# Kernel optimization log

Measured on AMD Instinct MI355X. Metric: run time of the kernel, lower is better.

Reference implementation:

```python
import jax, jax.numpy as jnp
import numpy as np

B, N, T, F_IN, K, NUM_CLASSES = 32, 62, 1024, 5, 9, 3
CH = [F_IN, 32, 64, 128]
STRIDES = [1, 2, 1]
EPS = 1e-5  # torch InstanceNorm2d default eps


def setup_inputs() -> dict:
    key = jax.random.key(0)
    ks = jax.random.split(key, 32)
    ctr = [0]
    def nxt():
        k = ks[ctr[0]]; ctr[0] += 1; return k
    def nrm(shape, fan_in):
        return jax.random.normal(nxt(), shape, dtype=jnp.float32) / np.float32(np.sqrt(fan_in))
    inp = {}
    inp["x"] = jax.random.normal(nxt(), (B, N, T, F_IN), dtype=jnp.float32)
    # frozen learned graph: symmetric, non-negative, sparse-ish, zero diagonal
    a = jax.random.uniform(nxt(), (N, N), dtype=jnp.float32)
    a = jnp.maximum(jnp.tanh(a + a.T), 0.0)
    a = jnp.where(a > 0.8, a, 0.0)
    inp["adj"] = a * (1.0 - jnp.eye(N, dtype=jnp.float32))
    for i in range(3):
        cin, cout = CH[i], CH[i + 1]
        inp[f"gcn_w{i}"] = nrm((cin, cout), cin)
        inp[f"gcn_b{i}"] = jnp.zeros((cout,), jnp.float32)
        inp[f"conv_w{i}"] = nrm((cout, cout, 1, K), cout * K)
        inp[f"conv_b{i}"] = jnp.zeros((cout,), jnp.float32)
        inp[f"res_w{i}"] = nrm((cout, cin, 1, 1), cin)
        inp[f"res_b{i}"] = jnp.zeros((cout,), jnp.float32)
    inp["attn_w1"] = nrm((128, 64), 128)
    inp["attn_b1"] = jnp.zeros((64,), jnp.float32)
    inp["attn_w2"] = nrm((64, 1), 64)
    inp["attn_b2"] = jnp.zeros((1,), jnp.float32)
    inp["fc_w"] = nrm((128, NUM_CLASSES), 128)
    inp["fc_b"] = jnp.zeros((NUM_CLASSES,), jnp.float32)
    return inp


def _instance_norm(x):
    # InstanceNorm2d, affine=False: normalize per (sample, channel) over (node, time)
    m = jnp.mean(x, axis=(2, 3), keepdims=True)
    v = jnp.mean(jnp.square(x - m), axis=(2, 3), keepdims=True)
    return (x - m) * jax.lax.rsqrt(v + EPS)


def _conv(x, w, b, stride, pad):
    y = jax.lax.conv_general_dilated(
        x, w, window_strides=(1, stride), padding=[(0, 0), (pad, pad)],
        dimension_numbers=("NCHW", "OIHW", "NCHW"))
    return y + b[None, :, None, None]


def _block(x, a_norm, wg, bg, wc, bc, wr, br, stride):
    # residual 1x1 conv (always present: in!=out for every block here)
    res = _conv(x, wr, br, stride, 0)
    # GCNConv over all (batch, time) slices at once: A_norm @ (X W) + b
    y = jnp.einsum("bfnt,fo->bont", x, wg)
    y = jnp.einsum("mn,bont->bomt", a_norm, y) + bg[None, :, None, None]
    # TCN: IN -> ReLU -> Conv(1,K) -> IN -> ReLU (dropout = identity in eval)
    y = jax.nn.relu(_instance_norm(y))
    y = _conv(y, wc, bc, stride, (K - 1) // 2)
    y = jax.nn.relu(_instance_norm(y))
    return jax.nn.relu(y + res)


def _forward(x, adj, params, attn_w1, attn_b1, attn_w2, attn_b2, fc_w, fc_b):
    # symmetric GCN normalization with self loops (PyG gcn_norm on dense support)
    a_hat = adj + jnp.eye(N, dtype=adj.dtype)
    d = jnp.sum(a_hat, axis=1)
    dinv = jnp.where(d > 0, jax.lax.rsqrt(jnp.maximum(d, EPS)), 0.0)
    a_norm = dinv[:, None] * a_hat * dinv[None, :]
    h = jnp.transpose(x, (0, 3, 1, 2))  # (B, F, N, T)
    for i in range(3):
        h = _block(h, a_norm, *params[i], STRIDES[i])
    h = jnp.transpose(jnp.mean(h, axis=2), (0, 2, 1))  # (B, T', 128)
    hid = jnp.tanh(h @ attn_w1 + attn_b1)
    score = (hid @ attn_w2)[..., 0] + attn_b2[0]      # (B, T')
    w = jax.nn.softmax(score, axis=1)
    feat = jnp.einsum("btf,bt->bf", h, w)
    logits = feat @ fc_w + fc_b
    return logits, adj


def reference(x, adj,
              gcn_w0, gcn_b0, conv_w0, conv_b0, res_w0, res_b0,
              gcn_w1, gcn_b1, conv_w1, conv_b1, res_w1, res_b1,
              gcn_w2, gcn_b2, conv_w2, conv_b2, res_w2, res_b2,
              attn_w1, attn_b1, attn_w2, attn_b2, fc_w, fc_b):
    params = [
        (gcn_w0, gcn_b0, conv_w0, conv_b0, res_w0, res_b0),
        (gcn_w1, gcn_b1, conv_w1, conv_b1, res_w1, res_b1),
        (gcn_w2, gcn_b2, conv_w2, conv_b2, res_w2, res_b2),
    ]
    return _forward(x, adj, params, attn_w1, attn_b1, attn_w2, attn_b2, fc_w, fc_b)
```

## Files before the change

kernel.cpp:

```cpp
#include <hip/hip_runtime.h>


#define NN 62
#define KK 9

typedef short s16x8 __attribute__((ext_vector_type(8)));
typedef float f32x4 __attribute__((ext_vector_type(4)));

__device__ __forceinline__ unsigned short f2bf(float f) {
  unsigned u = __builtin_bit_cast(unsigned, f);
  u += 0x7FFF + ((u >> 16) & 1);
  return (unsigned short)(u >> 16);
}
__device__ __forceinline__ float bf2f(unsigned short u) {
  unsigned v = ((unsigned)u) << 16;
  return __builtin_bit_cast(float, v);
}
__device__ __forceinline__ ushort4 pack4(float4 a) {
  return (ushort4){f2bf(a.x), f2bf(a.y), f2bf(a.z), f2bf(a.w)};
}

__global__ __launch_bounds__(256) void k_prep(const float* __restrict__ adj,
                                              float* __restrict__ a_norm,
                                              float* __restrict__ out_adj) {
  __shared__ float dinv[NN];
  int tid = threadIdx.x;
  if (tid < NN) {
    float s = 1.0f;
    for (int n = 0; n < NN; n++) s += adj[tid * NN + n];
    dinv[tid] = (s > 0.f) ? rsqrtf(fmaxf(s, 1e-5f)) : 0.f;
  }
  __syncthreads();
  for (int idx = tid; idx < NN * NN; idx += 256) {
    int m = idx / NN, n = idx - m * NN;
    float ah = adj[idx] + ((m == n) ? 1.f : 0.f);
    a_norm[idx] = dinv[m] * ah * dinv[n];
    out_adj[idx] = adj[idx];
  }
}

__global__ __launch_bounds__(256) void k_an(const float* __restrict__ a_norm,
                                            unsigned short* __restrict__ anf) {
  int idx = blockIdx.x * 256 + threadIdx.x;
  if (idx >= 4096) return;
  int j = idx & 7;
  int l = (idx >> 3) & 63;
  int rest = idx >> 9;
  int cb = rest & 1;
  int ob = rest >> 1;
  int m = ob * 16 + (l & 15);
  int n = cb * 32 + (l >> 4) * 8 + j;
  anf[idx] = (m < NN && n < NN) ? f2bf(a_norm[m * NN + n]) : (unsigned short)0;
}

__global__ __launch_bounds__(256) void k_wt(const float* __restrict__ wc,
                                            unsigned short* __restrict__ wf, int C) {
  int stride = gridDim.x * blockDim.x;
  int total = KK * C * C;
  int nCB = C / 32;
  for (int idx = blockIdx.x * blockDim.x + threadIdx.x; idx < total; idx += stride) {
    int j = idx & 7;
    int l = (idx >> 3) & 63;
    int rest = idx >> 9;
    int cb = rest % nCB;
    int rest2 = rest / nCB;
    int ob = rest2 % (C / 16);
    int k = rest2 / (C / 16);
    int o = ob * 16 + (l & 15);
    int ci = cb * 32 + (l >> 4) * 8 + j;
    wf[idx] = f2bf(wc[((size_t)o * C + ci) * KK + k]);
  }
}

__global__ __launch_bounds__(256) void k_wg(const float* __restrict__ gw,
                                            unsigned short* __restrict__ wgf,
                                            int CIN, int COUT, int KPAD) {
  int total = (COUT / 16) * (KPAD / 32) * 512;
  int stride = gridDim.x * blockDim.x;
  for (int idx = blockIdx.x * blockDim.x + threadIdx.x; idx < total; idx += stride) {
    int j = idx & 7;
    int l = (idx >> 3) & 63;
    int rest = idx >> 9;
    int cb = rest % (KPAD / 32);
    int ob = rest / (KPAD / 32);
    int o = ob * 16 + (l & 15);
    int f = cb * 32 + (l >> 4) * 8 + j;
    wgf[idx] = (f < CIN) ? f2bf(gw[(size_t)f * COUT + o]) : (unsigned short)0;
  }
}

__global__ __launch_bounds__(256) void k_wr(const float* __restrict__ wr,
                                            unsigned short* __restrict__ wrf,
                                            int CIN, int COUT, int KPAD) {
  int total = (COUT / 16) * (KPAD / 32) * 512;
  int stride = gridDim.x * blockDim.x;
  for (int idx = blockIdx.x * blockDim.x + threadIdx.x; idx < total; idx += stride) {
    int j = idx & 7;
    int l = (idx >> 3) & 63;
    int rest = idx >> 9;
    int cb = rest % (KPAD / 32);
    int ob = rest / (KPAD / 32);
    int o = ob * 16 + (l & 15);
    int f = cb * 32 + (l >> 4) * 8 + j;
    wrf[idx] = (f < CIN) ? f2bf(wr[(size_t)o * CIN + f]) : (unsigned short)0;
  }
}

__global__ __launch_bounds__(256) void k_xcast(const float* __restrict__ x,
                                               unsigned short* __restrict__ xb, int b0) {
  constexpr int TT2 = 256, TIN = 1024, CIN = 5;
  __shared__ float xt[TT2 * CIN];
  int t0 = blockIdx.x * TT2, n = blockIdx.y, bl = blockIdx.z;
  int tid = threadIdx.x;
  const float* xp = x + ((size_t)((b0 + bl) * NN + n) * TIN + t0) * CIN;
  for (int i = tid; i < TT2 * CIN; i += 256) xt[i] = xp[i];
  __syncthreads();
  for (int i = tid; i < CIN * TT2; i += 256) {
    int f = i / TT2, tl = i - f * TT2;
    xb[((size_t)bl * CIN + f) * NN * TIN + (size_t)n * TIN + t0 + tl] = f2bf(xt[tl * CIN + f]);
  }
}

template <int CIN, int TIN>
__global__ __launch_bounds__(256) void k_spatmma(const unsigned short* __restrict__ in,
                                                 const unsigned short* __restrict__ anf,
                                                 unsigned short* __restrict__ xs) {
  constexpr int BT = 256;
  constexpr int CP = 72;
  constexpr int BNP = BT + 8;
  constexpr int ZTSZ = BT * CP;
  constexpr int WLSZ = 4096;
  constexpr int OTSZ = 64 * BNP;
  constexpr int SH = (ZTSZ + WLSZ > OTSZ) ? ZTSZ + WLSZ : OTSZ;
  __shared__ unsigned short sh[SH];
  unsigned short* zt = sh;
  unsigned short* wl = sh + ZTSZ;

  int t0 = blockIdx.x * BT;
  int f = blockIdx.y;
  int bl = blockIdx.z;
  int tid = threadIdx.x;

  for (int i = tid * 4; i < WLSZ; i += 1024)
    *reinterpret_cast<ushort4*>(&wl[i]) = *reinterpret_cast<const ushort4*>(&anf[i]);

  const unsigned short* ib = in + ((size_t)bl * CIN + f) * (size_t)NN * TIN;
  for (int i = tid * 4; i < 64 * BT; i += 1024) {
    int n = i / BT, tl = i - n * BT;
    ushort4 u = {0, 0, 0, 0};
    if (n < NN) u = *reinterpret_cast<const ushort4*>(&ib[(size_t)n * TIN + t0 + tl]);
    unsigned short vv[4] = {u.x, u.y, u.z, u.w};
    int xo = ((tl >> 2) & 7) << 3;
#pragma unroll
    for (int j = 0; j < 4; j++) zt[(tl + j) * CP + (n ^ xo)] = vv[j];
  }
  __syncthreads();

  int w = tid >> 6;
  int lane = tid & 63;
  int lm = lane & 15, kh = lane >> 4;
  int col0 = w * 64;

  f32x4 acc[4][4];
#pragma unroll
  for (int mf = 0; mf < 4; mf++)
#pragma unroll
    for (int nf = 0; nf < 4; nf++) acc[mf][nf] = (f32x4){0.f, 0.f, 0.f, 0.f};

#pragma unroll
  for (int cb = 0; cb < 2; cb++) {
    s16x8 a[4], b[4];
#pragma unroll
    for (int mf = 0; mf < 4; mf++)
      a[mf] = *reinterpret_cast<const s16x8*>(&wl[(mf * 2 + cb) * 512 + lane * 8]);
#pragma unroll
    for (int nf = 0; nf < 4; nf++) {
      int col = col0 + nf * 16 + lm;
      int off = (cb * 32 + kh * 8) ^ (((col >> 2) & 7) << 3);
      b[nf] = *reinterpret_cast<const s16x8*>(&zt[col * CP + off]);
    }
#pragma unroll
    for (int mf = 0; mf < 4; mf++)
#pragma unroll
      for (int nf = 0; nf < 4; nf++)
        acc[mf][nf] = __builtin_amdgcn_mfma_f32_16x16x32_bf16(a[mf], b[nf], acc[mf][nf], 0, 0, 0);
  }

  __syncthreads();
  unsigned short* ot = sh;
#pragma unroll
  for (int mf = 0; mf < 4; mf++)
#pragma unroll
    for (int nf = 0; nf < 4; nf++) {
      int col = col0 + nf * 16 + lm;
#pragma unroll
      for (int rr = 0; rr < 4; rr++) {
        int m = mf * 16 + kh * 4 + rr;
        ot[m * BNP + col] = f2bf(acc[mf][nf][rr]);
      }
    }
  __syncthreads();
  for (int i = tid * 4; i < NN * BT; i += 1024) {
    int m = i / BT, col = i - m * BT;
    ushort4 v = *reinterpret_cast<const ushort4*>(&ot[m * BNP + col]);
    *reinterpret_cast<ushort4*>(&xs[(((size_t)bl * CIN + f) * NN + m) * TIN + t0 + col]) = v;
  }
}

template <int CIN, int COUT, int TIN>
__global__ __launch_bounds__(256) void k_wmixmma(const unsigned short* __restrict__ xs,
                                                 const unsigned short* __restrict__ wgf,
                                                 unsigned short* __restrict__ y,
                                                 float* __restrict__ part) {
  constexpr int S = NN * TIN;
  constexpr int KPAD = (CIN <= 32) ? 32 : 64;
  constexpr int CP = KPAD + 8;
  constexpr int BN = (COUT >= 128) ? 128 : 256;
  constexpr int BNP = BN + 8;
  constexpr int WM = (COUT >= 64) ? 2 : 1;
  constexpr int WN = 4 / WM;
  constexpr int MF = COUT / (16 * WM);
  constexpr int NF = BN / (16 * WN);
  constexpr int XM = (KPAD == 32) ? 3 : 7;
  constexpr int ZTSZ = BN * CP;
  constexpr int WLSZ = COUT * KPAD;
  constexpr int OTSZ = COUT * BNP;
  constexpr int SH = (ZTSZ + WLSZ > OTSZ) ? ZTSZ + WLSZ : OTSZ;
  __shared__ unsigned short sh[SH];
  unsigned short* zt = sh;
  unsigned short* wl = sh + ZTSZ;

  int s0 = blockIdx.x * BN;
  int bl = blockIdx.y;
  int tid = threadIdx.x;

  for (int i = tid * 4; i < WLSZ; i += 1024)
    *reinterpret_cast<ushort4*>(&wl[i]) = *reinterpret_cast<const ushort4*>(&wgf[i]);

  const unsigned short* xb = xs + (size_t)bl * CIN * S;
  for (int i = tid * 4; i < KPAD * BN; i += 1024) {
    int f = i / BN, sl = i - (i / BN) * BN;
    ushort4 u = {0, 0, 0, 0};
    if (f < CIN) u = *reinterpret_cast<const ushort4*>(&xb[(size_t)f * S + s0 + sl]);
    unsigned short vv[4] = {u.x, u.y, u.z, u.w};
#pragma unroll
    for (int j = 0; j < 4; j++) {
      int s_ = sl + j;
      zt[s_ * CP + (f ^ ((((s_) >> 2) & XM) << 3))] = vv[j];
    }
  }
  __syncthreads();

  int w = tid >> 6;
  int lane = tid & 63;
  int lm = lane & 15, kh = lane >> 4;
  int o0w = (w / WN) * (COUT / WM);
  int col0 = (w % WN) * (BN / WN);
  int obBase = o0w >> 4;

  f32x4 acc[MF][NF];
#pragma unroll
  for (int mf = 0; mf < MF; mf++)
#pragma unroll
    for (int nf = 0; nf < NF; nf++) acc[mf][nf] = (f32x4){0.f, 0.f, 0.f, 0.f};

#pragma unroll
  for (int cb = 0; cb < KPAD / 32; cb++) {
    s16x8 a[MF], b[NF];
#pragma unroll
    for (int mf = 0; mf < MF; mf++)
      a[mf] = *reinterpret_cast<const s16x8*>(&wl[((obBase + mf) * (KPAD / 32) + cb) * 512 + lane * 8]);
#pragma unroll
    for (int nf = 0; nf < NF; nf++) {
      int col = col0 + nf * 16 + lm;
      int off = (cb * 32 + kh * 8) ^ (((col >> 2) & XM) << 3);
      b[nf] = *reinterpret_cast<const s16x8*>(&zt[col * CP + off]);
    }
#pragma unroll
    for (int mf = 0; mf < MF; mf++)
#pragma unroll
      for (int nf = 0; nf < NF; nf++)
        acc[mf][nf] = __builtin_amdgcn_mfma_f32_16x16x32_bf16(a[mf], b[nf], acc[mf][nf], 0, 0, 0);
  }

  __syncthreads();
  unsigned short* ot = sh;
#pragma unroll
  for (int mf = 0; mf < MF; mf++)
#pragma unroll
    for (int nf = 0; nf < NF; nf++) {
      int col = col0 + nf * 16 + lm;
#pragma unroll
      for (int rr = 0; rr < 4; rr++) {
        int o = o0w + mf * 16 + kh * 4 + rr;
        ot[o * BNP + col] = f2bf(acc[mf][nf][rr]);
      }
    }
  __syncthreads();
  int NBLK = gridDim.x;
  constexpr int W = (BN / 4 < 64) ? BN / 4 : 64;
  for (int i = tid * 4; i < COUT * BN; i += 1024) {
    int o = i / BN, col = i - (i / BN) * BN;
    ushort4 v = *reinterpret_cast<const ushort4*>(&ot[o * BNP + col]);
    *reinterpret_cast<ushort4*>(&y[((size_t)bl * COUT + o) * S + s0 + col]) = v;
    float f0 = bf2f(v.x), f1 = bf2f(v.y), f2 = bf2f(v.z), f3 = bf2f(v.w);
    float s = f0 + f1 + f2 + f3;
    float s2 = f0 * f0 + f1 * f1 + f2 * f2 + f3 * f3;
    for (int off = W / 2; off; off >>= 1) {
      s += __shfl_down(s, off);
      s2 += __shfl_down(s2, off);
    }
    if ((tid & (W - 1)) == 0) {
      size_t po = (((size_t)bl * COUT + o) * NBLK + blockIdx.x) * 2;
      part[po] = s;
      part[po + 1] = s2;
    }
  }
}

__global__ __launch_bounds__(256) void k_statsR(const float* __restrict__ part,
                                                float* __restrict__ stats,
                                                int NBLK, float invS) {
  int c = blockIdx.x, C = gridDim.x, bl = blockIdx.y;
  const float* p = part + (((size_t)bl * C + c) * NBLK) * 2;
  float s = 0.f, s2 = 0.f;
  for (int i = threadIdx.x; i < NBLK; i += 256) {
    s += p[2 * i];
    s2 += p[2 * i + 1];
  }
  for (int off = 32; off; off >>= 1) {
    s += __shfl_down(s, off);
    s2 += __shfl_down(s2, off);
  }
  __shared__ float ls[4], ls2[4];
  int w = threadIdx.x >> 6;
  if ((threadIdx.x & 63) == 0) {
    ls[w] = s;
    ls2[w] = s2;
  }
  __syncthreads();
  if (threadIdx.x == 0) {
    float S1 = ls[0] + ls[1] + ls[2] + ls[3];
    float S2 = ls2[0] + ls2[1] + ls2[2] + ls2[3];
    float m = S1 * invS;
    float v = S2 * invS - m * m;
    stats[((size_t)bl * C + c) * 2 + 0] = m;
    stats[((size_t)bl * C + c) * 2 + 1] = rsqrtf(fmaxf(v, 0.f) + 1e-5f);
  }
}

template <int C, int TIN, int STRIDE, int BN>
__global__ __launch_bounds__(512) void k_convmma(const unsigned short* __restrict__ y,
                                                 const unsigned short* __restrict__ wf,
                                                 const float* __restrict__ statsY,
                                                 unsigned short* __restrict__ cbuf,
                                                 float* __restrict__ partC) {
  constexpr int TOUT = TIN / STRIDE;
  constexpr int SPAN = STRIDE * BN + 8;
  constexpr int CP = C + 8;
  constexpr int WM = (C >= 64) ? 2 : 1;
  constexpr int WN = 8 / WM;
  constexpr int MF = C / (16 * WM);
  constexpr int NF = BN / (16 * WN);
  constexpr int BNP = BN + 8;
  constexpr int XM = (C == 32) ? 3 : 7;
  constexpr int NCB = C / 32;
  constexpr int IT = KK * NCB;

  __shared__ unsigned short zt[SPAN * CP];
  static_assert(C * BNP <= SPAN * CP, "epilogue stage must fit in zt");

  int t0 = blockIdx.x * BN;
  int n = blockIdx.y;
  int bl = blockIdx.z;
  int tid = threadIdx.x;
  int tin0 = STRIDE * t0 - 4;

  int w = tid >> 6;
  int lane = tid & 63;
  int lm = lane & 15, kh = lane >> 4;
  int o0w = (w / WN) * (C / WM);
  int col0 = (w % WN) * (BN / WN);
  int obBase = o0w >> 4;

  const unsigned short* wp[MF];
  s16x8 acur[MF], anxt[MF];
#pragma unroll
  for (int mf = 0; mf < MF; mf++) {
    wp[mf] = wf + ((size_t)(obBase + mf) * NCB) * 512 + lane * 8;
    acur[mf] = *reinterpret_cast<const s16x8*>(wp[mf]);
  }

  const unsigned short* yb = y + ((size_t)bl * C) * NN * TIN + (size_t)n * TIN;
  const float* stY = statsY + (size_t)bl * 2 * C;
  for (int i = tid * 4; i < C * SPAN; i += 2048) {
    int ci = i / SPAN, r = i - ci * SPAN;
    int t = tin0 + r;
    const unsigned short* yrow = yb + (size_t)ci * NN * TIN;
    float m = stY[2 * ci], rs = stY[2 * ci + 1];
    float zv[4];
    if (t >= 0 && t + 4 <= TIN) {
      ushort4 u = *reinterpret_cast<const ushort4*>(&yrow[t]);
      zv[0] = fmaxf((bf2f(u.x) - m) * rs, 0.f);
      zv[1] = fmaxf((bf2f(u.y) - m) * rs, 0.f);
      zv[2] = fmaxf((bf2f(u.z) - m) * rs, 0.f);
      zv[3] = fmaxf((bf2f(u.w) - m) * rs, 0.f);
    } else {
#pragma unroll
      for (int j = 0; j < 4; j++) {
        int tj = t + j;
        zv[j] = (tj >= 0 && tj < TIN) ? fmaxf((bf2f(yrow[tj]) - m) * rs, 0.f) : 0.f;
      }
    }
    int xo = ((r >> 2) & XM) << 3;
#pragma unroll
    for (int j = 0; j < 4; j++) zt[(r + j) * CP + (ci ^ xo)] = f2bf(zv[j]);
  }

  f32x4 acc[MF][NF];
#pragma unroll
  for (int mf = 0; mf < MF; mf++)
#pragma unroll
    for (int nf = 0; nf < NF; nf++) acc[mf][nf] = (f32x4){0.f, 0.f, 0.f, 0.f};

  __syncthreads();

  for (int it = 0; it < IT; ++it) {
    int k = it / NCB, cb = it - (it / NCB) * NCB;
    if (it + 1 < IT) {
      int it2 = it + 1;
      int k2 = it2 / NCB, cb2 = it2 - (it2 / NCB) * NCB;
#pragma unroll
      for (int mf = 0; mf < MF; mf++)
        anxt[mf] = *reinterpret_cast<const s16x8*>(
            &wf[((((size_t)k2 * (C / 16) + obBase + mf) * NCB + cb2) << 9) + lane * 8]);
    }
    s16x8 b[NF];
#pragma unroll
    for (int nf = 0; nf < NF; nf++) {
      int col = col0 + nf * 16 + lm;
      int r = STRIDE * col + k;
      int off = (cb * 32 + kh * 8) ^ (((r >> 2) & XM) << 3);
      b[nf] = *reinterpret_cast<const s16x8*>(&zt[r * CP + off]);
    }
#pragma unroll
    for (int mf = 0; mf < MF; mf++)
#pragma unroll
      for (int nf = 0; nf < NF; nf++)
        acc[mf][nf] = __builtin_amdgcn_mfma_f32_16x16x32_bf16(acur[mf], b[nf], acc[mf][nf], 0, 0, 0);
    if (it + 1 < IT) {
#pragma unroll
      for (int mf = 0; mf < MF; mf++) acur[mf] = anxt[mf];
    }
  }

  __syncthreads();
  unsigned short* ot = zt;
#pragma unroll
  for (int mf = 0; mf < MF; mf++)
#pragma unroll
    for (int nf = 0; nf < NF; nf++) {
      int col = col0 + nf * 16 + lm;
#pragma unroll
      for (int rr = 0; rr < 4; rr++) {
        int o = o0w + mf * 16 + kh * 4 + rr;
        ot[o * BNP + col] = f2bf(acc[mf][nf][rr]);
      }
    }
  __syncthreads();
  int pb = blockIdx.y * gridDim.x + blockIdx.x;
  constexpr int W = (BN / 4 < 64) ? BN / 4 : 64;
  for (int i = tid * 4; i < C * BN; i += 2048) {
    int o = i / BN, col = i - (i / BN) * BN;
    ushort4 v = *reinterpret_cast<const ushort4*>(&ot[o * BNP + col]);
    *reinterpret_cast<ushort4*>(&cbuf[(((size_t)bl * C + o) * NN + n) * TOUT + t0 + col]) = v;
    float f0 = bf2f(v.x), f1 = bf2f(v.y), f2 = bf2f(v.z), f3 = bf2f(v.w);
    float s = f0 + f1 + f2 + f3;
    float s2 = f0 * f0 + f1 * f1 + f2 * f2 + f3 * f3;
    for (int off = W / 2; off; off >>= 1) {
      s += __shfl_down(s, off);
      s2 += __shfl_down(s2, off);
    }
    if ((tid & (W - 1)) == 0) {
      size_t po = (((size_t)bl * C + o) * 248 + pb) * 2;
      partC[po] = s;
      partC[po + 1] = s2;
    }
  }
}

template <int CIN, int COUT, int TOUT, int STRIDE>
__global__ __launch_bounds__(256) void k_postmma(const unsigned short* __restrict__ cbuf,
                                                 const float* __restrict__ statsC,
                                                 const unsigned short* __restrict__ in,
                                                 const unsigned short* __restrict__ wrf,
                                                 const float* __restrict__ br,
                                                 unsigned short* __restrict__ out) {
  constexpr int BN = 128;
  constexpr int TIN_ = TOUT * STRIDE;
  constexpr int KPAD = (CIN <= 32) ? 32 : 64;
  constexpr int CP = KPAD + 8;
  constexpr int BNP = BN + 8;
  constexpr int MF = (COUT >= 64) ? COUT / 32 : 1;
  constexpr int NF = 4;
  constexpr int XM = (KPAD == 32) ? 3 : 7;
  constexpr int ZTSZ = BN * CP;
  constexpr int WLSZ = COUT * KPAD;
  constexpr int OTSZ = COUT * BNP;
  constexpr int SH = (ZTSZ + WLSZ > OTSZ) ? ZTSZ + WLSZ : OTSZ;
  __shared__ unsigned short sh[SH];
  __shared__ float stL[2 * COUT];
  __shared__ float brL[COUT];
  unsigned short* zt = sh;
  unsigned short* wl = sh + ZTSZ;

  int t0 = blockIdx.x * BN;
  int n = blockIdx.y;
  int bl = blockIdx.z;
  int tid = threadIdx.x;

  for (int i = tid; i < 2 * COUT; i += 256) stL[i] = statsC[(size_t)bl * 2 * COUT + i];
  if (tid < COUT) brL[tid] = br[tid];

  for (int i = tid * 4; i < WLSZ; i += 1024)
    *reinterpret_cast<ushort4*>(&wl[i]) = *reinterpret_cast<const ushort4*>(&wrf[i]);

  const unsigned short* ib = in + ((size_t)bl * CIN) * NN * TIN_ + (size_t)n * TIN_;
  for (int i = tid * 4; i < KPAD * BN; i += 1024) {
    int f = i / BN, sl = i - (i / BN) * BN;
    unsigned short vv[4] = {0, 0, 0, 0};
    if (f < CIN) {
      const unsigned short* row = ib + (size_t)f * NN * TIN_;
      if (STRIDE == 1) {
        ushort4 u = *reinterpret_cast<const ushort4*>(&row[t0 + sl]);
        vv[0] = u.x; vv[1] = u.y; vv[2] = u.z; vv[3] = u.w;
      } else {
        ushort4 u0 = *reinterpret_cast<const ushort4*>(&row[2 * (t0 + sl)]);
        ushort4 u1 = *reinterpret_cast<const ushort4*>(&row[2 * (t0 + sl) + 4]);
        vv[0] = u0.x; vv[1] = u0.z; vv[2] = u1.x; vv[3] = u1.z;
      }
    }
#pragma unroll
    for (int j = 0; j < 4; j++) {
      int s_ = sl + j;
      zt[s_ * CP + (f ^ ((((s_) >> 2) & XM) << 3))] = vv[j];
    }
  }
  __syncthreads();

  int w = tid >> 6;
  int lane = tid & 63;
  int lm = lane & 15, kh = lane >> 4;
  int o0w = (w / 2) * (COUT / 2);
  int col0 = (w % 2) * 64;
  int obBase = o0w >> 4;

  f32x4 acc[MF][NF];
#pragma unroll
  for (int mf = 0; mf < MF; mf++)
#pragma unroll
    for (int nf = 0; nf < NF; nf++) acc[mf][nf] = (f32x4){0.f, 0.f, 0.f, 0.f};

#pragma unroll
  for (int cb = 0; cb < KPAD / 32; cb++) {
    s16x8 a[MF], b[NF];
#pragma unroll
    for (int mf = 0; mf < MF; mf++)
      a[mf] = *reinterpret_cast<const s16x8*>(&wl[((obBase + mf) * (KPAD / 32) + cb) * 512 + lane * 8]);
#pragma unroll
    for (int nf = 0; nf < NF; nf++) {
      int col = col0 + nf * 16 + lm;
      int off = (cb * 32 + kh * 8) ^ (((col >> 2) & XM) << 3);
      b[nf] = *reinterpret_cast<const s16x8*>(&zt[col * CP + off]);
    }
#pragma unroll
    for (int mf = 0; mf < MF; mf++)
#pragma unroll
      for (int nf = 0; nf < NF; nf++)
        acc[mf][nf] = __builtin_amdgcn_mfma_f32_16x16x32_bf16(a[mf], b[nf], acc[mf][nf], 0, 0, 0);
  }

  __syncthreads();
  unsigned short* ot = sh;
#pragma unroll
  for (int mf = 0; mf < MF; mf++)
#pragma unroll
    for (int nf = 0; nf < NF; nf++) {
      int col = col0 + nf * 16 + lm;
#pragma unroll
      for (int rr = 0; rr < 4; rr++) {
        int o = o0w + mf * 16 + kh * 4 + rr;
        ot[o * BNP + col] = f2bf(acc[mf][nf][rr]);
      }
    }
  __syncthreads();
  for (int i = tid * 4; i < COUT * BN; i += 1024) {
    int o = i / BN, col = i - (i / BN) * BN;
    ushort4 rv = *reinterpret_cast<const ushort4*>(&ot[o * BNP + col]);
    ushort4 cv = *reinterpret_cast<const ushort4*>(&cbuf[(((size_t)bl * COUT + o) * NN + n) * TOUT + t0 + col]);
    float m = stL[2 * o], rs = stL[2 * o + 1], bb = brL[o];
    ushort4 ov;
    float v0 = fmaxf((bf2f(cv.x) - m) * rs, 0.f) + bf2f(rv.x) + bb;
    float v1 = fmaxf((bf2f(cv.y) - m) * rs, 0.f) + bf2f(rv.y) + bb;
    float v2 = fmaxf((bf2f(cv.z) - m) * rs, 0.f) + bf2f(rv.z) + bb;
    float v3 = fmaxf((bf2f(cv.w) - m) * rs, 0.f) + bf2f(rv.w) + bb;
    ov.x = f2bf(fmaxf(v0, 0.f));
    ov.y = f2bf(fmaxf(v1, 0.f));
    ov.z = f2bf(fmaxf(v2, 0.f));
    ov.w = f2bf(fmaxf(v3, 0.f));
    *reinterpret_cast<ushort4*>(&out[(((size_t)bl * COUT + o) * NN + n) * TOUT + t0 + col]) = ov;
  }
}

__global__ __launch_bounds__(256) void k_pool(const unsigned short* __restrict__ src,
                                              float* __restrict__ pooled, int b0) {
  constexpr int CP2 = 128, TPZ = 512;
  int t = blockIdx.x * 64 + (threadIdx.x & 63);
  int c = blockIdx.y * 4 + (threadIdx.x >> 6);
  int bl = blockIdx.z;
  const unsigned short* p = src + ((size_t)bl * CP2 + c) * NN * TPZ + t;
  float s = 0.f;
  for (int n = 0; n < NN; n++) s += bf2f(p[(size_t)n * TPZ]);
  pooled[((size_t)(b0 + bl) * TPZ + t) * CP2 + c] = s * (1.f / NN);
}

__global__ __launch_bounds__(128) void k_attn1(const float* __restrict__ pooled,
                                               const float* __restrict__ w1,
                                               const float* __restrict__ b1,
                                               const float* __restrict__ w2,
                                               const float* __restrict__ b2v,
                                               float* __restrict__ score) {
  __shared__ float w1L[128 * 64];
  __shared__ float w2L[64];
  __shared__ float b1L[64];
  int b = blockIdx.y;
  int t = blockIdx.x * 128 + threadIdx.x;
  int tid = threadIdx.x;
  for (int i = tid; i < 128 * 64; i += 128) w1L[i] = w1[i];
  if (tid < 64) {
    w2L[tid] = w2[tid];
    b1L[tid] = b1[tid];
  }
  __syncthreads();
  float hid[64];
#pragma unroll
  for (int j = 0; j < 64; j++) hid[j] = b1L[j];
  const float* pv = &pooled[((size_t)b * 512 + t) * 128];
  for (int c = 0; c < 128; c++) {
    float xv = pv[c];
#pragma unroll
    for (int j = 0; j < 64; j++) hid[j] += xv * w1L[c * 64 + j];
  }
  float s = b2v[0];
#pragma unroll
  for (int j = 0; j < 64; j++) s += tanhf(hid[j]) * w2L[j];
  score[(size_t)b * 512 + t] = s;
}

__global__ __launch_bounds__(256) void k_attn2(const float* __restrict__ score,
                                               float* __restrict__ wgt) {
  __shared__ float sc[512];
  __shared__ float red[4];
  int b = blockIdx.x;
  int tid = threadIdx.x;
  for (int t = tid; t < 512; t += 256) sc[t] = score[(size_t)b * 512 + t];
  __syncthreads();
  float mx = -1e30f;
  for (int t = tid; t < 512; t += 256) mx = fmaxf(mx, sc[t]);
  for (int off = 32; off; off >>= 1) mx = fmaxf(mx, __shfl_down(mx, off));
  if ((tid & 63) == 0) red[tid >> 6] = mx;
  __syncthreads();
  mx = fmaxf(fmaxf(red[0], red[1]), fmaxf(red[2], red[3]));
  __syncthreads();
  float sum = 0.f;
  for (int t = tid; t < 512; t += 256) {
    float e = expf(sc[t] - mx);
    sc[t] = e;
    sum += e;
  }
  for (int off = 32; off; off >>= 1) sum += __shfl_down(sum, off);
  if ((tid & 63) == 0) red[tid >> 6] = sum;
  __syncthreads();
  float inv = 1.f / (red[0] + red[1] + red[2] + red[3]);
  for (int t = tid; t < 512; t += 256) wgt[(size_t)b * 512 + t] = sc[t] * inv;
}

__global__ __launch_bounds__(256) void k_feat2(const float* __restrict__ pooled,
                                               const float* __restrict__ wgt,
                                               float* __restrict__ featb) {
  __shared__ float sh[16][17];
  int b = blockIdx.y;
  int c0 = blockIdx.x * 16;
  int cl = threadIdx.x & 15, tlane = threadIdx.x >> 4;
  float s = 0.f;
  for (int t = tlane; t < 512; t += 16)
    s += pooled[((size_t)b * 512 + t) * 128 + c0 + cl] * wgt[(size_t)b * 512 + t];
  sh[tlane][cl] = s;
  __syncthreads();
  if (threadIdx.x < 16) {
    float a = 0.f;
    for (int q = 0; q < 16; q++) a += sh[q][threadIdx.x];
    featb[(size_t)b * 128 + c0 + threadIdx.x] = a;
  }
}

__global__ __launch_bounds__(128) void k_logits(const float* __restrict__ featb,
                                                const float* __restrict__ fcw,
                                                const float* __restrict__ fcb,
                                                float* __restrict__ out) {
  __shared__ float fL[128];
  int b = blockIdx.x;
  fL[threadIdx.x] = featb[(size_t)b * 128 + threadIdx.x];
  __syncthreads();
  if (threadIdx.x < 3) {
    float l = fcb[threadIdx.x];
    for (int cc = 0; cc < 128; cc++) l += fL[cc] * fcw[cc * 3 + threadIdx.x];
    out[(size_t)b * 3 + threadIdx.x] = l;
  }
}

extern "C" void kernel_launch(void* const* d_in, const int* in_sizes, int n_in,
                              void* d_out, int out_size, void* d_ws, size_t ws_size,
                              hipStream_t stream) {
  (void)in_sizes; (void)n_in; (void)out_size;
  const float* x = (const float*)d_in[0];
  const float* adj = (const float*)d_in[1];
  const float* gw0 = (const float*)d_in[2];
  const float* cw0 = (const float*)d_in[4];
  const float* rw0 = (const float*)d_in[6];
  const float* rb0 = (const float*)d_in[7];
  const float* gw1 = (const float*)d_in[8];
  const float* cw1 = (const float*)d_in[10];
  const float* rw1 = (const float*)d_in[12];
  const float* rb1 = (const float*)d_in[13];
  const float* gw2 = (const float*)d_in[14];
  const float* cw2 = (const float*)d_in[16];
  const float* rw2 = (const float*)d_in[18];
  const float* rb2 = (const float*)d_in[19];
  const float* aw1 = (const float*)d_in[20];
  const float* ab1 = (const float*)d_in[21];
  const float* aw2 = (const float*)d_in[22];
  const float* ab2 = (const float*)d_in[23];
  const float* fcw = (const float*)d_in[24];
  const float* fcb = (const float*)d_in[25];
  float* out = (float*)d_out;
  float* ws = (float*)d_ws;

  float* a_norm = ws;
  unsigned short* wk0 = (unsigned short*)(a_norm + 3844);
  unsigned short* wk1 = (unsigned short*)(a_norm + 8452);
  unsigned short* wk2 = (unsigned short*)(a_norm + 26884);
  unsigned short* wg0f = (unsigned short*)(a_norm + 100612);
  unsigned short* wg1f = (unsigned short*)(a_norm + 101124);
  unsigned short* wg2f = (unsigned short*)(a_norm + 102148);
  unsigned short* anf = (unsigned short*)(a_norm + 106244);
  unsigned short* wr0f = (unsigned short*)(a_norm + 108292);
  unsigned short* wr1f = (unsigned short*)(a_norm + 108804);
  unsigned short* wr2f = (unsigned short*)(a_norm + 109828);
  float* pooled = a_norm + 113924;
  float* scoreb = pooled + 2097152;
  float* wgtA = scoreb + 16384;
  float* featb = wgtA + 16384;
  float* chunk_base = featb + 4096;
  size_t shared_floats = (size_t)(chunk_base - ws);

  const size_t PS_BUF = 2031616;
  const size_t PS_P1 = 131072;
  const size_t PS_P2 = 65536;
  const size_t per_sample = 3 * PS_BUF + PS_P1 + PS_P2 + 512;

  size_t avail = ws_size / sizeof(float);
  long cap = 1;
  if (avail > shared_floats) cap = (long)((avail - shared_floats) / per_sample);
  int Bc = (int)cap;
  if (Bc < 1) Bc = 1;
  if (Bc > 32) Bc = 32;

  k_prep<<<dim3(1), dim3(256), 0, stream>>>(adj, a_norm, out + 96);
  k_an<<<dim3(16), dim3(256), 0, stream>>>(a_norm, anf);
  k_wt<<<dim3(64), dim3(256), 0, stream>>>(cw0, wk0, 32);
  k_wt<<<dim3(160), dim3(256), 0, stream>>>(cw1, wk1, 64);
  k_wt<<<dim3(576), dim3(256), 0, stream>>>(cw2, wk2, 128);
  k_wg<<<dim3(4), dim3(256), 0, stream>>>(gw0, wg0f, 5, 32, 32);
  k_wg<<<dim3(8), dim3(256), 0, stream>>>(gw1, wg1f, 32, 64, 32);
  k_wg<<<dim3(32), dim3(256), 0, stream>>>(gw2, wg2f, 64, 128, 64);
  k_wr<<<dim3(4), dim3(256), 0, stream>>>(rw0, wr0f, 5, 32, 32);
  k_wr<<<dim3(8), dim3(256), 0, stream>>>(rw1, wr1f, 32, 64, 32);
  k_wr<<<dim3(32), dim3(256), 0, stream>>>(rw2, wr2f, 64, 128, 64);

  float* sp1 = chunk_base;
  float* sp2 = sp1 + (size_t)Bc * PS_P1;
  float* stY = sp2 + (size_t)Bc * PS_P2;
  float* stC = stY + (size_t)Bc * 256;
  float* B1 = stC + (size_t)Bc * 256;
  float* B2 = B1 + (size_t)Bc * PS_BUF;
  float* B3 = B2 + (size_t)Bc * PS_BUF;

  for (int b0 = 0; b0 < 32; b0 += Bc) {
    int bc = (32 - b0 < Bc) ? (32 - b0) : Bc;
    unsigned short* B1u = (unsigned short*)B1;
    unsigned short* B2u = (unsigned short*)B2;
    unsigned short* B3u = (unsigned short*)B3;

    k_xcast<<<dim3(4, NN, bc), dim3(256), 0, stream>>>(x, B1u, b0);
    k_spatmma<5, 1024><<<dim3(4, 5, bc), dim3(256), 0, stream>>>(B1u, anf, B2u);
    k_wmixmma<5, 32, 1024><<<dim3(248, bc), dim3(256), 0, stream>>>(B2u, wg0f, B3u, sp1);
    k_statsR<<<dim3(32, bc), dim3(256), 0, stream>>>(sp1, stY, 248, 1.f / 63488.f);
    k_convmma<32, 1024, 1, 256><<<dim3(4, NN, bc), dim3(512), 0, stream>>>(B3u, wk0, stY, B2u, sp2);
    k_statsR<<<dim3(32, bc), dim3(256), 0, stream>>>(sp2, stC, 248, 1.f / 63488.f);
    k_postmma<5, 32, 1024, 1><<<dim3(8, NN, bc), dim3(256), 0, stream>>>(
        B2u, stC, B1u, wr0f, rb0, B3u);

    k_spatmma<32, 1024><<<dim3(4, 32, bc), dim3(256), 0, stream>>>(B3u, anf, B1u);
    k_wmixmma<32, 64, 1024><<<dim3(248, bc), dim3(256), 0, stream>>>(B1u, wg1f, B2u, sp1);
    k_statsR<<<dim3(64, bc), dim3(256), 0, stream>>>(sp1, stY, 248, 1.f / 63488.f);
    k_convmma<64, 1024, 2, 128><<<dim3(4, NN, bc), dim3(512), 0, stream>>>(B2u, wk1, stY, B1u, sp2);
    k_statsR<<<dim3(64, bc), dim3(256), 0, stream>>>(sp2, stC, 248, 1.f / 31744.f);
    k_postmma<32, 64, 512, 2><<<dim3(4, NN, bc), dim3(256), 0, stream>>>(
        B1u, stC, B3u, wr1f, rb1, B2u);

    k_spatmma<64, 512><<<dim3(2, 64, bc), dim3(256), 0, stream>>>(B2u, anf, B3u);
    k_wmixmma<64, 128, 512><<<dim3(248, bc), dim3(256), 0, stream>>>(B3u, wg2f, B1u, sp1);
    k_statsR<<<dim3(128, bc), dim3(256), 0, stream>>>(sp1, stY, 248, 1.f / 31744.f);
    k_convmma<128, 512, 1, 128><<<dim3(4, NN, bc), dim3(512), 0, stream>>>(B1u, wk2, stY, B3u, sp2);
    k_statsR<<<dim3(128, bc), dim3(256), 0, stream>>>(sp2, stC, 248, 1.f / 31744.f);
    k_postmma<64, 128, 512, 1><<<dim3(4, NN, bc), dim3(256), 0, stream>>>(
        B3u, stC, B2u, wr2f, rb2, B1u);

    k_pool<<<dim3(8, 32, bc), dim3(256), 0, stream>>>(B1u, pooled, b0);
  }

  k_attn1<<<dim3(4, 32), dim3(128), 0, stream>>>(pooled, aw1, ab1, aw2, ab2, scoreb);
  k_attn2<<<dim3(32), dim3(256), 0, stream>>>(scoreb, wgtA);
  k_feat2<<<dim3(8, 32), dim3(256), 0, stream>>>(pooled, wgtA, featb);
  k_logits<<<dim3(32), dim3(128), 0, stream>>>(featb, fcw, fcb, out);
}
```

Baseline: 2.024 ms.

## Fuse stats reduction into consumer kernels and merge weight-prep launches

Removes the six k_statsR launches by having each k_convmma and k_postmma block reduce the 248 partial sums per channel itself, straight from the partial buffers. It also merges the ten small weight and adjacency repacking kernels into one 2D-grid launch that dispatches on blockIdx.y. This cuts launch count and the serialized gaps between tiny kernels. The cost is that every consumer block now repeats a serial 248-element reduction per channel in a single thread, which is redundant work and adds latency at the start of each block.

```diff
diff --git a/kernel.cpp b/kernel.cpp
--- a/kernel.cpp
+++ b/kernel.cpp
@@ -3,6 +3,7 @@
 
 #define NN 62
 #define KK 9
+#define NPB 248
 
 typedef short s16x8 __attribute__((ext_vector_type(8)));
 typedef float f32x4 __attribute__((ext_vector_type(4)));
@@ -39,70 +40,86 @@
   }
 }
 
-__global__ __launch_bounds__(256) void k_an(const float* __restrict__ a_norm,
-                                            unsigned short* __restrict__ anf) {
-  int idx = blockIdx.x * 256 + threadIdx.x;
-  if (idx >= 4096) return;
+__device__ __forceinline__ void wt_fill(const float* __restrict__ wc,
+                                        unsigned short* __restrict__ wf, int C, int idx) {
+  int total = KK * C * C;
+  if (idx >= total) return;
+  int nCB = C / 32;
   int j = idx & 7;
   int l = (idx >> 3) & 63;
   int rest = idx >> 9;
-  int cb = rest & 1;
-  int ob = rest >> 1;
-  int m = ob * 16 + (l & 15);
-  int n = cb * 32 + (l >> 4) * 8 + j;
-  anf[idx] = (m < NN && n < NN) ? f2bf(a_norm[m * NN + n]) : (unsigned short)0;
-}
-
-__global__ __launch_bounds__(256) void k_wt(const float* __restrict__ wc,
-                                            unsigned short* __restrict__ wf, int C) {
-  int stride = gridDim.x * blockDim.x;
-  int total = KK * C * C;
-  int nCB = C / 32;
-  for (int idx = blockIdx.x * blockDim.x + threadIdx.x; idx < total; idx += stride) {
-    int j = idx & 7;
-    int l = (idx >> 3) & 63;
-    int rest = idx >> 9;
-    int cb = rest % nCB;
-    int rest2 = rest / nCB;
-    int ob = rest2 % (C / 16);
-    int k = rest2 / (C / 16);
-    int o = ob * 16 + (l & 15);
-    int ci = cb * 32 + (l >> 4) * 8 + j;
-    wf[idx] = f2bf(wc[((size_t)o * C + ci) * KK + k]);
-  }
-}
-
-__global__ __launch_bounds__(256) void k_wg(const float* __restrict__ gw,
-                                            unsigned short* __restrict__ wgf,
-                                            int CIN, int COUT, int KPAD) {
+  int cb = rest % nCB;
+  int rest2 = rest / nCB;
+  int ob = rest2 % (C / 16);
+  int k = rest2 / (C / 16);
+  int o = ob * 16 + (l & 15);
+  int ci = cb * 32 + (l >> 4) * 8 + j;
+  wf[idx] = f2bf(wc[((size_t)o * C + ci) * KK + k]);
+}
+__device__ __forceinline__ void wg_fill(const float* __restrict__ gw,
+                                        unsigned short* __restrict__ wgf,
+                                        int CIN, int COUT, int KPAD, int idx) {
   int total = (COUT / 16) * (KPAD / 32) * 512;
-  int stride = gridDim.x * blockDim.x;
-  for (int idx = blockIdx.x * blockDim.x + threadIdx.x; idx < total; idx += stride) {
-    int j = idx & 7;
-    int l = (idx >> 3) & 63;
-    int rest = idx >> 9;
-    int cb = rest % (KPAD / 32);
-    int ob = rest / (KPAD / 32);
-    int o = ob * 16 + (l & 15);
-    int f = cb * 32 + (l >> 4) * 8 + j;
-    wgf[idx] = (f < CIN) ? f2bf(gw[(size_t)f * COUT + o]) : (unsigned short)0;
-  }
-}
-
-__global__ __launch_bounds__(256) void k_wr(const float* __restrict__ wr,
-                                            unsigned short* __restrict__ wrf,
-                                            int CIN, int COUT, int KPAD) {
+  if (idx >= total) return;
+  int j = idx & 7;
+  int l = (idx >> 3) & 63;
+  int rest = idx >> 9;
+  int cb = rest % (KPAD / 32);
+  int ob = rest / (KPAD / 32);
+  int o = ob * 16 + (l & 15);
+  int f = cb * 32 + (l >> 4) * 8 + j;
+  wgf[idx] = (f < CIN) ? f2bf(gw[(size_t)f * COUT + o]) : (unsigned short)0;
+}
+__device__ __forceinline__ void wr_fill(const float* __restrict__ wr,
+                                        unsigned short* __restrict__ wrf,
+                                        int CIN, int COUT, int KPAD, int idx) {
   int total = (COUT / 16) * (KPAD / 32) * 512;
-  int stride = gridDim.x * blockDim.x;
-  for (int idx = blockIdx.x * blockDim.x + threadIdx.x; idx < total; idx += stride) {
-    int j = idx & 7;
-    int l = (idx >> 3) & 63;
-    int rest = idx >> 9;
-    int cb = rest % (KPAD / 32);
-    int ob = rest / (KPAD / 32);
-    int o = ob * 16 + (l & 15);
-    int f = cb * 32 + (l >> 4) * 8 + j;
-    wrf[idx] = (f < CIN) ? f2bf(wr[(size_t)o * CIN + f]) : (unsigned short)0;
+  if (idx >= total) return;
+  int j = idx & 7;
+  int l = (idx >> 3) & 63;
+  int rest = idx >> 9;
+  int cb = rest % (KPAD / 32);
+  int ob = rest / (KPAD / 32);
+  int o = ob * 16 + (l & 15);
+  int f = cb * 32 + (l >> 4) * 8 + j;
+  wrf[idx] = (f < CIN) ? f2bf(wr[(size_t)o * CIN + f]) : (unsigned short)0;
+}
+
+__global__ __launch_bounds__(256) void k_wall(
+    const float* __restrict__ a_norm, unsigned short* __restrict__ anf,
+    const float* __restrict__ cw0, unsigned short* __restrict__ wk0,
+    const float* __restrict__ cw1, unsigned short* __restrict__ wk1,
+    const float* __restrict__ cw2, unsigned short* __restrict__ wk2,
+    const float* __restrict__ gw0, unsigned short* __restrict__ wg0f,
+    const float* __restrict__ gw1, unsigned short* __restrict__ wg1f,
+    const float* __restrict__ gw2, unsigned short* __restrict__ wg2f,
+    const float* __restrict__ rw0, unsigned short* __restrict__ wr0f,
+    const float* __restrict__ rw1, unsigned short* __restrict__ wr1f,
+    const float* __restrict__ rw2, unsigned short* __restrict__ wr2f) {
+  int idx = blockIdx.x * 256 + threadIdx.x;
+  switch (blockIdx.y) {
+    case 0: {
+      if (idx < 4096) {
+        int j = idx & 7;
+        int l = (idx >> 3) & 63;
+        int rest = idx >> 9;
+        int cb = rest & 1;
+        int ob = rest >> 1;
+        int m = ob * 16 + (l & 15);
+        int n = cb * 32 + (l >> 4) * 8 + j;
+        anf[idx] = (m < NN && n < NN) ? f2bf(a_norm[m * NN + n]) : (unsigned short)0;
+      }
+      break;
+    }
+    case 1: wt_fill(cw0, wk0, 32, idx); break;
+    case 2: wt_fill(cw1, wk1, 64, idx); break;
+    case 3: wt_fill(cw2, wk2, 128, idx); break;
+    case 4: wg_fill(gw0, wg0f, 5, 32, 32, idx); break;
+    case 5: wg_fill(gw1, wg1f, 32, 64, 32, idx); break;
+    case 6: wg_fill(gw2, wg2f, 64, 128, 64, idx); break;
+    case 7: wr_fill(rw0, wr0f, 5, 32, 32, idx); break;
+    case 8: wr_fill(rw1, wr1f, 32, 64, 32, idx); break;
+    case 9: wr_fill(rw2, wr2f, 64, 128, 64, idx); break;
   }
 }
 
@@ -318,41 +335,11 @@
   }
 }
 
-__global__ __launch_bounds__(256) void k_statsR(const float* __restrict__ part,
-                                                float* __restrict__ stats,
-                                                int NBLK, float invS) {
-  int c = blockIdx.x, C = gridDim.x, bl = blockIdx.y;
-  const float* p = part + (((size_t)bl * C + c) * NBLK) * 2;
-  float s = 0.f, s2 = 0.f;
-  for (int i = threadIdx.x; i < NBLK; i += 256) {
-    s += p[2 * i];
-    s2 += p[2 * i + 1];
-  }
-  for (int off = 32; off; off >>= 1) {
-    s += __shfl_down(s, off);
-    s2 += __shfl_down(s2, off);
-  }
-  __shared__ float ls[4], ls2[4];
-  int w = threadIdx.x >> 6;
-  if ((threadIdx.x & 63) == 0) {
-    ls[w] = s;
-    ls2[w] = s2;
-  }
-  __syncthreads();
-  if (threadIdx.x == 0) {
-    float S1 = ls[0] + ls[1] + ls[2] + ls[3];
-    float S2 = ls2[0] + ls2[1] + ls2[2] + ls2[3];
-    float m = S1 * invS;
-    float v = S2 * invS - m * m;
-    stats[((size_t)bl * C + c) * 2 + 0] = m;
-    stats[((size_t)bl * C + c) * 2 + 1] = rsqrtf(fmaxf(v, 0.f) + 1e-5f);
-  }
-}
-
 template <int C, int TIN, int STRIDE, int BN>
 __global__ __launch_bounds__(512) void k_convmma(const unsigned short* __restrict__ y,
                                                  const unsigned short* __restrict__ wf,
-                                                 const float* __restrict__ statsY,
+                                                 const float* __restrict__ partY,
+                                                 float invS,
                                                  unsigned short* __restrict__ cbuf,
                                                  float* __restrict__ partC) {
   constexpr int TOUT = TIN / STRIDE;
@@ -368,6 +355,7 @@
   constexpr int IT = KK * NCB;
 
   __shared__ unsigned short zt[SPAN * CP];
+  __shared__ float stYL[2 * C];
   static_assert(C * BNP <= SPAN * CP, "epilogue stage must fit in zt");
 
   int t0 = blockIdx.x * BN;
@@ -391,13 +379,26 @@
     acur[mf] = *reinterpret_cast<const s16x8*>(wp[mf]);
   }
 
+  for (int c = tid; c < C; c += 512) {
+    const float* p = partY + ((size_t)bl * C + c) * (NPB * 2);
+    float s = 0.f, s2 = 0.f;
+    for (int i = 0; i < NPB * 2; i += 2) {
+      s += p[i];
+      s2 += p[i + 1];
+    }
+    float m = s * invS;
+    float v = s2 * invS - m * m;
+    stYL[2 * c] = m;
+    stYL[2 * c + 1] = rsqrtf(fmaxf(v, 0.f) + 1e-5f);
+  }
+  __syncthreads();
+
   const unsigned short* yb = y + ((size_t)bl * C) * NN * TIN + (size_t)n * TIN;
-  const float* stY = statsY + (size_t)bl * 2 * C;
   for (int i = tid * 4; i < C * SPAN; i += 2048) {
     int ci = i / SPAN, r = i - ci * SPAN;
     int t = tin0 + r;
     const unsigned short* yrow = yb + (size_t)ci * NN * TIN;
-    float m = stY[2 * ci], rs = stY[2 * ci + 1];
+    float m = stYL[2 * ci], rs = stYL[2 * ci + 1];
     float zv[4];
     if (t >= 0 && t + 4 <= TIN) {
       ushort4 u = *reinterpret_cast<const ushort4*>(&yrow[t]);
@@ -482,7 +483,7 @@
       s2 += __shfl_down(s2, off);
     }
     if ((tid & (W - 1)) == 0) {
-      size_t po = (((size_t)bl * C + o) * 248 + pb) * 2;
+      size_t po = (((size_t)bl * C + o) * NPB + pb) * 2;
       partC[po] = s;
       partC[po + 1] = s2;
     }
@@ -491,7 +492,8 @@
 
 template <int CIN, int COUT, int TOUT, int STRIDE>
 __global__ __launch_bounds__(256) void k_postmma(const unsigned short* __restrict__ cbuf,
-                                                 const float* __restrict__ statsC,
+                                                 const float* __restrict__ partC,
+                                                 float invS,
                                                  const unsigned short* __restrict__ in,
                                                  const unsigned short* __restrict__ wrf,
                                                  const float* __restrict__ br,
@@ -519,7 +521,18 @@
   int bl = blockIdx.z;
   int tid = threadIdx.x;
 
-  for (int i = tid; i < 2 * COUT; i += 256) stL[i] = statsC[(size_t)bl * 2 * COUT + i];
+  for (int c = tid; c < COUT; c += 256) {
+    const float* p = partC + ((size_t)bl * COUT + c) * (NPB * 2);
+    float s = 0.f, s2 = 0.f;
+    for (int i = 0; i < NPB * 2; i += 2) {
+      s += p[i];
+      s2 += p[i + 1];
+    }
+    float m = s * invS;
+    float v = s2 * invS - m * m;
+    stL[2 * c] = m;
+    stL[2 * c + 1] = rsqrtf(fmaxf(v, 0.f) + 1e-5f);
+  }
   if (tid < COUT) brL[tid] = br[tid];
 
   for (int i = tid * 4; i < WLSZ; i += 1024)
@@ -777,22 +790,13 @@
   if (Bc > 32) Bc = 32;
 
   k_prep<<<dim3(1), dim3(256), 0, stream>>>(adj, a_norm, out + 96);
-  k_an<<<dim3(16), dim3(256), 0, stream>>>(a_norm, anf);
-  k_wt<<<dim3(64), dim3(256), 0, stream>>>(cw0, wk0, 32);
-  k_wt<<<dim3(160), dim3(256), 0, stream>>>(cw1, wk1, 64);
-  k_wt<<<dim3(576), dim3(256), 0, stream>>>(cw2, wk2, 128);
-  k_wg<<<dim3(4), dim3(256), 0, stream>>>(gw0, wg0f, 5, 32, 32);
-  k_wg<<<dim3(8), dim3(256), 0, stream>>>(gw1, wg1f, 32, 64, 32);
-  k_wg<<<dim3(32), dim3(256), 0, stream>>>(gw2, wg2f, 64, 128, 64);
-  k_wr<<<dim3(4), dim3(256), 0, stream>>>(rw0, wr0f, 5, 32, 32);
-  k_wr<<<dim3(8), dim3(256), 0, stream>>>(rw1, wr1f, 32, 64, 32);
-  k_wr<<<dim3(32), dim3(256), 0, stream>>>(rw2, wr2f, 64, 128, 64);
+  k_wall<<<dim3(576, 10), dim3(256), 0, stream>>>(
+      a_norm, anf, cw0, wk0, cw1, wk1, cw2, wk2,
+      gw0, wg0f, gw1, wg1f, gw2, wg2f, rw0, wr0f, rw1, wr1f, rw2, wr2f);
 
   float* sp1 = chunk_base;
   float* sp2 = sp1 + (size_t)Bc * PS_P1;
-  float* stY = sp2 + (size_t)Bc * PS_P2;
-  float* stC = stY + (size_t)Bc * 256;
-  float* B1 = stC + (size_t)Bc * 256;
+  float* B1 = sp2 + (size_t)Bc * PS_P2;
   float* B2 = B1 + (size_t)Bc * PS_BUF;
   float* B3 = B2 + (size_t)Bc * PS_BUF;
 
@@ -805,27 +809,24 @@
     k_xcast<<<dim3(4, NN, bc), dim3(256), 0, stream>>>(x, B1u, b0);
     k_spatmma<5, 1024><<<dim3(4, 5, bc), dim3(256), 0, stream>>>(B1u, anf, B2u);
     k_wmixmma<5, 32, 1024><<<dim3(248, bc), dim3(256), 0, stream>>>(B2u, wg0f, B3u, sp1);
-    k_statsR<<<dim3(32, bc), dim3(256), 0, stream>>>(sp1, stY, 248, 1.f / 63488.f);
-    k_convmma<32, 1024, 1, 256><<<dim3(4, NN, bc), dim3(512), 0, stream>>>(B3u, wk0, stY, B2u, sp2);
-    k_statsR<<<dim3(32, bc), dim3(256), 0, stream>>>(sp2, stC, 248, 1.f / 63488.f);
+    k_convmma<32, 1024, 1, 256><<<dim3(4, NN, bc), dim3(512), 0, stream>>>(
+        B3u, wk0, sp1, 1.f / 63488.f, B2u, sp2);
     k_postmma<5, 32, 1024, 1><<<dim3(8, NN, bc), dim3(256), 0, stream>>>(
-        B2u, stC, B1u, wr0f, rb0, B3u);
+        B2u, sp2, 1.f / 63488.f, B1u, wr0f, rb0, B3u);
 
     k_spatmma<32, 1024><<<dim3(4, 32, bc), dim3(256), 0, stream>>>(B3u, anf, B1u);
     k_wmixmma<32, 64, 1024><<<dim3(248, bc), dim3(256), 0, stream>>>(B1u, wg1f, B2u, sp1);
-    k_statsR<<<dim3(64, bc), dim3(256), 0, stream>>>(sp1, stY, 248, 1.f / 63488.f);
-    k_convmma<64, 1024, 2, 128><<<dim3(4, NN, bc), dim3(512), 0, stream>>>(B2u, wk1, stY, B1u, sp2);
-    k_statsR<<<dim3(64, bc), dim3(256), 0, stream>>>(sp2, stC, 248, 1.f / 31744.f);
+    k_convmma<64, 1024, 2, 128><<<dim3(4, NN, bc), dim3(512), 0, stream>>>(
+        B2u, wk1, sp1, 1.f / 63488.f, B1u, sp2);
     k_postmma<32, 64, 512, 2><<<dim3(4, NN, bc), dim3(256), 0, stream>>>(
-        B1u, stC, B3u, wr1f, rb1, B2u);
+        B1u, sp2, 1.f / 31744.f, B3u, wr1f, rb1, B2u);
 
     k_spatmma<64, 512><<<dim3(2, 64, bc), dim3(256), 0, stream>>>(B2u, anf, B3u);
     k_wmixmma<64, 128, 512><<<dim3(248, bc), dim3(256), 0, stream>>>(B3u, wg2f, B1u, sp1);
-    k_statsR<<<dim3(128, bc), dim3(256), 0, stream>>>(sp1, stY, 248, 1.f / 31744.f);
-    k_convmma<128, 512, 1, 128><<<dim3(4, NN, bc), dim3(512), 0, stream>>>(B1u, wk2, stY, B3u, sp2);
-    k_statsR<<<dim3(128, bc), dim3(256), 0, stream>>>(sp2, stC, 248, 1.f / 31744.f);
+    k_convmma<128, 512, 1, 128><<<dim3(4, NN, bc), dim3(512), 0, stream>>>(
+        B1u, wk2, sp1, 1.f / 31744.f, B3u, sp2);
     k_postmma<64, 128, 512, 1><<<dim3(4, NN, bc), dim3(256), 0, stream>>>(
-        B3u, stC, B2u, wr2f, rb2, B1u);
+        B3u, sp2, 1.f / 31744.f, B2u, wr2f, rb2, B1u);
 
     k_pool<<<dim3(8, 32, bc), dim3(256), 0, stream>>>(B1u, pooled, b0);
   }
```

New measurement: 2.748 ms. 1.36x slower.
